# Kernel optimization log

Hardware: AMD Instinct MI355X
Metric: run time of the kernel (lower is better)

Reference implementation:

```python
import jax, jax.numpy as jnp
import numpy as np

B, S, D = 2, 2048, 1024
H = 16
HD = D // H


def setup_inputs() -> dict:
    key = jax.random.key(0)
    k1, k2, k3 = jax.random.split(key, 3)
    x = jax.random.normal(k1, (B, S, D), dtype=jnp.float32)
    # nn.Linear(d, 3d, bias=False): weight [3d, d]; y = x @ W.T
    w_qkv = jax.random.normal(k2, (3 * D, D), dtype=jnp.float32) * (D ** -0.5)
    w_out = jax.random.normal(k3, (D, D), dtype=jnp.float32) * (D ** -0.5)
    return {"x": x, "w_qkv": w_qkv, "w_out": w_out}


def reference(x, w_qkv, w_out):
    batch, seq_len, _ = x.shape
    qkv = jnp.einsum('bsd,ed->bse', x, w_qkv)  # [B,S,3D]
    q, k, v = jnp.split(qkv, 3, axis=-1)
    # [B,S,D] -> [B,H,S,HD]
    def heads(t):
        return t.reshape(batch, seq_len, H, HD).transpose(0, 2, 1, 3)
    q, k, v = heads(q), heads(k), heads(v)
    scale = HD ** -0.5
    attn = jnp.einsum('bhqd,bhkd->bhqk', q, k) * scale  # [B,H,S,S]
    causal = jnp.triu(jnp.ones((seq_len, seq_len), dtype=bool), k=1)
    attn = jnp.where(causal, -jnp.inf, attn)
    attn = jax.nn.softmax(attn, axis=-1)
    out = jnp.einsum('bhqk,bhkd->bhqd', attn, v)  # [B,H,S,HD]
    out = out.transpose(0, 2, 1, 3).reshape(batch, seq_len, D)
    return jnp.einsum('bsd,ed->bse', out, w_out)
```

## Files before the change

kernel.cpp:

```cpp
#include <hip/hip_runtime.h>

#define NUM_B 2
#define SEQ   2048
#define DIM   1024
#define NH    16
#define HD    64

typedef __attribute__((ext_vector_type(8))) short short8;
typedef __attribute__((ext_vector_type(4))) float floatx4;
typedef unsigned short us;

#define SOFTMAX_SHIFT 12.0f

__device__ __forceinline__ us f2bf(float f) {
    unsigned u = __float_as_uint(f);
    u += 0x7fffu + ((u >> 16) & 1u);
    return (us)(u >> 16);
}
__device__ __forceinline__ us f2bf_t(float f) {
    return (us)(__float_as_uint(f) >> 16);
}

#define GLD16(gptr, lptr) __builtin_amdgcn_global_load_lds( \
    (__attribute__((address_space(1))) unsigned int*)(gptr), \
    (__attribute__((address_space(3))) unsigned int*)(lptr), 16, 0, 0)

__global__ __launch_bounds__(256) void cast_all(
    const float* __restrict__ x, const float* __restrict__ wq,
    const float* __restrict__ wo, us* __restrict__ xb,
    us* __restrict__ wqb, us* __restrict__ wob)
{
    int i = blockIdx.x * 256 + threadIdx.x;
    const float* src; us* dst; int off;
    if (i < 524288)      { src = x;  dst = xb;  off = i; }
    else if (i < 917504) { src = wq; dst = wqb; off = i - 524288; }
    else                 { src = wo; dst = wob; off = i - 917504; }
    const float4* p = (const float4*)src + (size_t)off * 2;
    float4 f0 = p[0];
    float4 f1 = p[1];
    short8 v;
    v[0] = (short)f2bf(f0.x); v[1] = (short)f2bf(f0.y);
    v[2] = (short)f2bf(f0.z); v[3] = (short)f2bf(f0.w);
    v[4] = (short)f2bf(f1.x); v[5] = (short)f2bf(f1.y);
    v[6] = (short)f2bf(f1.z); v[7] = (short)f2bf(f1.w);
    *(short8*)(dst + (size_t)off * 8) = v;
}

__global__ __launch_bounds__(256, 2) void gemm_qkv(
    const us* __restrict__ A, const us* __restrict__ Bw,
    us* __restrict__ qb, us* __restrict__ kb, us* __restrict__ vt)
{
    __shared__ us As[128 * 64];
    __shared__ us Bs[128 * 64];
    const int t = threadIdx.x;
    const int lane = t & 63, w = t >> 6;
    const int l16 = lane & 15, quad = lane >> 4;
    const int wr = (w >> 1) * 64, wc = (w & 1) * 64;
    const int m0 = blockIdx.y * 128, n0 = blockIdx.x * 128;
    const int srow = lane >> 3;
    const int soff = ((lane & 7) ^ srow) << 3;
    const int rsw  = l16 & 7;

    floatx4 acc[4][4];
    #pragma unroll
    for (int i = 0; i < 4; ++i)
        #pragma unroll
        for (int j = 0; j < 4; ++j) acc[i][j] = (floatx4){0.f, 0.f, 0.f, 0.f};

    for (int k0 = 0; k0 < DIM; k0 += 64) {
        #pragma unroll
        for (int c = 0; c < 4; ++c) {
            int chunk = w * 4 + c;
            int row = chunk * 8 + srow;
            GLD16(A  + (size_t)(m0 + row) * DIM + k0 + soff, &As[chunk * 512]);
            GLD16(Bw + (size_t)(n0 + row) * DIM + k0 + soff, &Bs[chunk * 512]);
        }
        __syncthreads();
        #pragma unroll
        for (int s = 0; s < 2; ++s) {
            short8 af[4], bf[4];
            #pragma unroll
            for (int i = 0; i < 4; ++i)
                af[i] = *(const short8*)&As[(wr + i * 16 + l16) * 64 + (((s * 4 + quad) ^ rsw) << 3)];
            #pragma unroll
            for (int j = 0; j < 4; ++j)
                bf[j] = *(const short8*)&Bs[(wc + j * 16 + l16) * 64 + (((s * 4 + quad) ^ rsw) << 3)];
            #pragma unroll
            for (int i = 0; i < 4; ++i)
                #pragma unroll
                for (int j = 0; j < 4; ++j)
                    acc[i][j] = __builtin_amdgcn_mfma_f32_16x16x32_bf16(af[i], bf[j], acc[i][j], 0, 0, 0);
        }
        __syncthreads();
    }

    #pragma unroll
    for (int i = 0; i < 4; ++i) {
        #pragma unroll
        for (int j = 0; j < 4; ++j) {
            int e = n0 + wc + j * 16 + l16;
            int which = e >> 10;
            int h  = (e >> 6) & 15;
            int hd = e & 63;
            float sc = (which == 0) ? 0.125f : 1.0f;
            #pragma unroll
            for (int r = 0; r < 4; ++r) {
                int m = m0 + wr + i * 16 + quad * 4 + r;
                int b = m >> 11, s = m & 2047;
                us v = f2bf(acc[i][j][r] * sc);
                if (which == 0)      qb[((size_t)((b * NH + h) * SEQ + s) << 6) + hd] = v;
                else if (which == 1) kb[((size_t)((b * NH + h) * SEQ + s) << 6) + hd] = v;
                else                 vt[((size_t)((b * NH + h) * HD + hd) << 11) + s] = v;
            }
        }
    }
}

__global__ __launch_bounds__(256, 2) void gemm_out(
    const us* __restrict__ A, const us* __restrict__ Bw, float* __restrict__ outp)
{
    __shared__ us As[64 * 64];
    __shared__ us Bs[128 * 64];
    const int t = threadIdx.x;
    const int lane = t & 63, w = t >> 6;
    const int l16 = lane & 15, quad = lane >> 4;
    const int wr = (w >> 1) * 32, wc = (w & 1) * 64;
    const int m0 = blockIdx.y * 64, n0 = blockIdx.x * 128;
    const int srow = lane >> 3;
    const int soff = ((lane & 7) ^ srow) << 3;
    const int rsw  = l16 & 7;

    floatx4 acc[2][4];
    #pragma unroll
    for (int i = 0; i < 2; ++i)
        #pragma unroll
        for (int j = 0; j < 4; ++j) acc[i][j] = (floatx4){0.f, 0.f, 0.f, 0.f};

    for (int k0 = 0; k0 < DIM; k0 += 64) {
        #pragma unroll
        for (int c = 0; c < 2; ++c) {
            int chunk = w * 2 + c;
            int row = chunk * 8 + srow;
            GLD16(A + (size_t)(m0 + row) * DIM + k0 + soff, &As[chunk * 512]);
        }
        #pragma unroll
        for (int c = 0; c < 4; ++c) {
            int chunk = w * 4 + c;
            int row = chunk * 8 + srow;
            GLD16(Bw + (size_t)(n0 + row) * DIM + k0 + soff, &Bs[chunk * 512]);
        }
        __syncthreads();
        #pragma unroll
        for (int s = 0; s < 2; ++s) {
            short8 af[2], bf[4];
            #pragma unroll
            for (int i = 0; i < 2; ++i)
                af[i] = *(const short8*)&As[(wr + i * 16 + l16) * 64 + (((s * 4 + quad) ^ rsw) << 3)];
            #pragma unroll
            for (int j = 0; j < 4; ++j)
                bf[j] = *(const short8*)&Bs[(wc + j * 16 + l16) * 64 + (((s * 4 + quad) ^ rsw) << 3)];
            #pragma unroll
            for (int i = 0; i < 2; ++i)
                #pragma unroll
                for (int j = 0; j < 4; ++j)
                    acc[i][j] = __builtin_amdgcn_mfma_f32_16x16x32_bf16(af[i], bf[j], acc[i][j], 0, 0, 0);
        }
        __syncthreads();
    }

    #pragma unroll
    for (int i = 0; i < 2; ++i)
        #pragma unroll
        for (int j = 0; j < 4; ++j) {
            int n = n0 + wc + j * 16 + l16;
            #pragma unroll
            for (int r = 0; r < 4; ++r) {
                int m = m0 + wr + i * 16 + quad * 4 + r;
                outp[(size_t)m * DIM + n] = acc[i][j][r];
            }
        }
}

__global__ __launch_bounds__(256, 4) void attn(
    const us* __restrict__ qb, const us* __restrict__ kb,
    const us* __restrict__ vt, us* __restrict__ ob)
{
    __shared__ us Ks[64 * 64];
    __shared__ us Vs[64 * 64];
    __shared__ us Ps[4 * 16 * 72];
    const int t = threadIdx.x;
    const int lane = t & 63, w = t >> 6;
    const int l16 = lane & 15, quad = lane >> 4;
    const int idx = blockIdx.x;
    const int qt = 31 - (idx >> 5);
    const int bh = idx & 31;
    const int b = bh >> 4, h = bh & 15;
    const int q0 = qt << 6;
    const int r0 = q0 + w * 16;
    const int rowb = r0 + quad * 4;
    const size_t base = (size_t)bh * SEQ * HD;
    const us* qbh = qb + base;
    const us* kbh = kb + base;
    const us* vth = vt + base;
    us* Pp = Ps + w * 16 * 72;
    const int srow = lane >> 3;
    const int soff = ((lane & 7) ^ srow) << 3;
    const int rsw  = l16 & 7;

    short8 qa[2];
    #pragma unroll
    for (int s = 0; s < 2; ++s)
        qa[s] = *(const short8*)(qbh + (size_t)(r0 + l16) * HD + s * 32 + quad * 8);

    floatx4 o[4];
    #pragma unroll
    for (int j = 0; j < 4; ++j) o[j] = (floatx4){0.f, 0.f, 0.f, 0.f};
    float lrow[4] = {0.f, 0.f, 0.f, 0.f};

    for (int kt = 0; kt <= qt; ++kt) {
        const int j0 = kt << 6;
        #pragma unroll
        for (int c = 0; c < 2; ++c) {
            int chunk = w * 2 + c;
            int row = chunk * 8 + srow;
            GLD16(kbh + (size_t)(j0 + row) * HD + soff, &Ks[chunk * 512]);
            GLD16(vth + (size_t)row * SEQ + j0 + soff, &Vs[chunk * 512]);
        }
        __syncthreads();

        floatx4 sf[4];
        #pragma unroll
        for (int j = 0; j < 4; ++j)
            sf[j] = (floatx4){-SOFTMAX_SHIFT, -SOFTMAX_SHIFT, -SOFTMAX_SHIFT, -SOFTMAX_SHIFT};
        #pragma unroll
        for (int s = 0; s < 2; ++s)
            #pragma unroll
            for (int j = 0; j < 4; ++j) {
                short8 kf = *(const short8*)&Ks[(j * 16 + l16) * 64 + (((s * 4 + quad) ^ rsw) << 3)];
                sf[j] = __builtin_amdgcn_mfma_f32_16x16x32_bf16(qa[s], kf, sf[j], 0, 0, 0);
            }

        float p[4][4];
        #pragma unroll
        for (int j = 0; j < 4; ++j)
            #pragma unroll
            for (int r = 0; r < 4; ++r) p[j][r] = sf[j][r];

        if (kt == qt) {
            #pragma unroll
            for (int j = 0; j < 4; ++j) {
                int colg = j0 + j * 16 + l16;
                #pragma unroll
                for (int r = 0; r < 4; ++r)
                    if (colg > rowb + r) p[j][r] = -1e30f;
            }
        }

        #pragma unroll
        for (int j = 0; j < 4; ++j)
            #pragma unroll
            for (int r = 0; r < 4; ++r) {
                p[j][r] = __expf(p[j][r]);
                Pp[(quad * 4 + r) * 72 + j * 16 + l16] = f2bf_t(p[j][r]);
            }
        #pragma unroll
        for (int r = 0; r < 4; ++r)
            lrow[r] += (p[0][r] + p[1][r]) + (p[2][r] + p[3][r]);

        #pragma unroll
        for (int s = 0; s < 2; ++s) {
            short8 pf = *(const short8*)&Pp[l16 * 72 + s * 32 + quad * 8];
            #pragma unroll
            for (int j = 0; j < 4; ++j) {
                short8 vf = *(const short8*)&Vs[(j * 16 + l16) * 64 + (((s * 4 + quad) ^ rsw) << 3)];
                o[j] = __builtin_amdgcn_mfma_f32_16x16x32_bf16(pf, vf, o[j], 0, 0, 0);
            }
        }
        __syncthreads();
    }

    #pragma unroll
    for (int r = 0; r < 4; ++r) {
        float l = lrow[r];
        l += __shfl_xor(l, 1);
        l += __shfl_xor(l, 2);
        l += __shfl_xor(l, 4);
        l += __shfl_xor(l, 8);
        float inv = 1.0f / l;
        #pragma unroll
        for (int j = 0; j < 4; ++j) {
            float val = o[j][r] * inv;
            ob[(size_t)(b * SEQ + rowb + r) * DIM + h * HD + j * 16 + l16] = f2bf(val);
        }
    }
}

extern "C" void kernel_launch(void* const* d_in, const int* in_sizes, int n_in,
                              void* d_out, int out_size, void* d_ws, size_t ws_size,
                              hipStream_t stream) {
    const float* x     = (const float*)d_in[0];
    const float* w_qkv = (const float*)d_in[1];
    const float* w_out = (const float*)d_in[2];
    float* out = (float*)d_out;
    us* ws = (us*)d_ws;

    const size_t M1 = (size_t)1024 * 1024;
    us* xb  = ws;
    us* wqb = xb  + 4 * M1;
    us* wob = wqb + 3 * M1;
    us* qb  = wob + 1 * M1;
    us* kb  = qb  + 4 * M1;
    us* vt  = kb  + 4 * M1;
    us* obf = vt  + 4 * M1;

    cast_all<<<4096, 256, 0, stream>>>(x, w_qkv, w_out, xb, wqb, wob);
    gemm_qkv<<<dim3(24, 32), 256, 0, stream>>>(xb, wqb, qb, kb, vt);
    attn<<<1024, 256, 0, stream>>>(qb, kb, vt, obf);
    gemm_out<<<dim3(8, 64), 256, 0, stream>>>(obf, wob, out);
}
```

Measured before the change: 173.0 us.

## Rewrite attention with 32x32x16 MFMA and 128-row query tiles

The attention kernel now gives each block 128 query rows instead of 64, and each wave handles 32 rows using 32x32x16 bf16 MFMA in place of 16x16x32. Every K/V tile staged in LDS is therefore reused by twice as many query rows, and fewer MFMA instructions are issued per tile. Causal work is balanced by pairing tile indices across the two halves of the grid. The costs are a larger P buffer with a new swizzle, more accumulator registers with occupancy lowered to 2 blocks per CU, half as many blocks, and masking that now covers the last two key tiles.

```diff
diff --git a/kernel.cpp b/kernel.cpp
--- a/kernel.cpp
+++ b/kernel.cpp
@@ -7,7 +7,9 @@
 #define HD    64
 
 typedef __attribute__((ext_vector_type(8))) short short8;
+typedef __attribute__((ext_vector_type(4))) short short4v;
 typedef __attribute__((ext_vector_type(4))) float floatx4;
+typedef __attribute__((ext_vector_type(16))) float floatx16;
 typedef unsigned short us;
 
 #define SOFTMAX_SHIFT 12.0f
@@ -181,43 +183,46 @@
         }
 }
 
-__global__ __launch_bounds__(256, 4) void attn(
+__global__ __launch_bounds__(256, 2) void attn(
     const us* __restrict__ qb, const us* __restrict__ kb,
     const us* __restrict__ vt, us* __restrict__ ob)
 {
     __shared__ us Ks[64 * 64];
     __shared__ us Vs[64 * 64];
-    __shared__ us Ps[4 * 16 * 72];
+    __shared__ us Ps[4 * 32 * 64];
     const int t = threadIdx.x;
     const int lane = t & 63, w = t >> 6;
-    const int l16 = lane & 15, quad = lane >> 4;
+    const int l31 = lane & 31, hi = lane >> 5;
     const int idx = blockIdx.x;
-    const int qt = 31 - (idx >> 5);
-    const int bh = idx & 31;
+    const int ii = idx & 255;
+    const int Qi = (idx >> 8) ? (ii >> 5) : (15 - (ii >> 5));
+    const int bh = ii & 31;
     const int b = bh >> 4, h = bh & 15;
-    const int q0 = qt << 6;
-    const int r0 = q0 + w * 16;
-    const int rowb = r0 + quad * 4;
+    const int q0 = Qi << 7;
+    const int myrow = q0 + ((l31 >> 4) << 6) + (w << 4) + (l31 & 15);
     const size_t base = (size_t)bh * SEQ * HD;
     const us* qbh = qb + base;
     const us* kbh = kb + base;
     const us* vth = vt + base;
-    us* Pp = Ps + w * 16 * 72;
+    us* Pp = Ps + w * 32 * 64;
     const int srow = lane >> 3;
     const int soff = ((lane & 7) ^ srow) << 3;
-    const int rsw  = l16 & 7;
-
-    short8 qa[2];
-    #pragma unroll
-    for (int s = 0; s < 2; ++s)
-        qa[s] = *(const short8*)(qbh + (size_t)(r0 + l16) * HD + s * 32 + quad * 8);
-
-    floatx4 o[4];
-    #pragma unroll
-    for (int j = 0; j < 4; ++j) o[j] = (floatx4){0.f, 0.f, 0.f, 0.f};
-    float lrow[4] = {0.f, 0.f, 0.f, 0.f};
-
-    for (int kt = 0; kt <= qt; ++kt) {
+    const int xsw = l31 & 7;
+    const int nk = 2 * Qi + 2;
+
+    short8 qa[4];
+    #pragma unroll
+    for (int s = 0; s < 4; ++s)
+        qa[s] = *(const short8*)(qbh + (size_t)myrow * HD + s * 16 + hi * 8);
+
+    floatx16 o[2];
+    #pragma unroll
+    for (int db = 0; db < 2; ++db)
+        #pragma unroll
+        for (int e = 0; e < 16; ++e) o[db][e] = 0.f;
+    float lsum = 0.f;
+
+    for (int kt = 0; kt < nk; ++kt) {
         const int j0 = kt << 6;
         #pragma unroll
         for (int c = 0; c < 2; ++c) {
@@ -228,69 +233,72 @@
         }
         __syncthreads();
 
-        floatx4 sf[4];
-        #pragma unroll
-        for (int j = 0; j < 4; ++j)
-            sf[j] = (floatx4){-SOFTMAX_SHIFT, -SOFTMAX_SHIFT, -SOFTMAX_SHIFT, -SOFTMAX_SHIFT};
-        #pragma unroll
-        for (int s = 0; s < 2; ++s)
-            #pragma unroll
-            for (int j = 0; j < 4; ++j) {
-                short8 kf = *(const short8*)&Ks[(j * 16 + l16) * 64 + (((s * 4 + quad) ^ rsw) << 3)];
-                sf[j] = __builtin_amdgcn_mfma_f32_16x16x32_bf16(qa[s], kf, sf[j], 0, 0, 0);
-            }
-
-        float p[4][4];
-        #pragma unroll
-        for (int j = 0; j < 4; ++j)
-            #pragma unroll
-            for (int r = 0; r < 4; ++r) p[j][r] = sf[j][r];
-
-        if (kt == qt) {
-            #pragma unroll
-            for (int j = 0; j < 4; ++j) {
-                int colg = j0 + j * 16 + l16;
+        floatx16 sfa[2];
+        #pragma unroll
+        for (int kb2 = 0; kb2 < 2; ++kb2)
+            #pragma unroll
+            for (int e = 0; e < 16; ++e) sfa[kb2][e] = -SOFTMAX_SHIFT;
+        #pragma unroll
+        for (int kb2 = 0; kb2 < 2; ++kb2)
+            #pragma unroll
+            for (int s = 0; s < 4; ++s) {
+                short8 kf = *(const short8*)&Ks[(kb2 * 32 + l31) * 64 + (((s * 2 + hi) ^ xsw) << 3)];
+                sfa[kb2] = __builtin_amdgcn_mfma_f32_32x32x16_bf16(kf, qa[s], sfa[kb2], 0, 0, 0);
+            }
+
+        if (kt >= nk - 2) {
+            #pragma unroll
+            for (int kb2 = 0; kb2 < 2; ++kb2)
                 #pragma unroll
-                for (int r = 0; r < 4; ++r)
-                    if (colg > rowb + r) p[j][r] = -1e30f;
-            }
-        }
-
-        #pragma unroll
-        for (int j = 0; j < 4; ++j)
-            #pragma unroll
-            for (int r = 0; r < 4; ++r) {
-                p[j][r] = __expf(p[j][r]);
-                Pp[(quad * 4 + r) * 72 + j * 16 + l16] = f2bf_t(p[j][r]);
-            }
-        #pragma unroll
-        for (int r = 0; r < 4; ++r)
-            lrow[r] += (p[0][r] + p[1][r]) + (p[2][r] + p[3][r]);
-
-        #pragma unroll
-        for (int s = 0; s < 2; ++s) {
-            short8 pf = *(const short8*)&Pp[l16 * 72 + s * 32 + quad * 8];
-            #pragma unroll
-            for (int j = 0; j < 4; ++j) {
-                short8 vf = *(const short8*)&Vs[(j * 16 + l16) * 64 + (((s * 4 + quad) ^ rsw) << 3)];
-                o[j] = __builtin_amdgcn_mfma_f32_16x16x32_bf16(pf, vf, o[j], 0, 0, 0);
-            }
-        }
-        __syncthreads();
-    }
-
-    #pragma unroll
-    for (int r = 0; r < 4; ++r) {
-        float l = lrow[r];
-        l += __shfl_xor(l, 1);
-        l += __shfl_xor(l, 2);
-        l += __shfl_xor(l, 4);
-        l += __shfl_xor(l, 8);
-        float inv = 1.0f / l;
-        #pragma unroll
-        for (int j = 0; j < 4; ++j) {
-            float val = o[j][r] * inv;
-            ob[(size_t)(b * SEQ + rowb + r) * DIM + h * HD + j * 16 + l16] = f2bf(val);
+                for (int reg = 0; reg < 16; ++reg) {
+                    int key = j0 + kb2 * 32 + (reg & 3) + ((reg >> 2) << 3) + (hi << 2);
+                    if (key > myrow) sfa[kb2][reg] = -1e30f;
+                }
+        }
+
+        #pragma unroll
+        for (int kb2 = 0; kb2 < 2; ++kb2) {
+            float pv[16];
+            #pragma unroll
+            for (int reg = 0; reg < 16; ++reg) {
+                pv[reg] = __expf(sfa[kb2][reg]);
+                lsum += pv[reg];
+            }
+            #pragma unroll
+            for (int rg = 0; rg < 4; ++rg) {
+                short4v pk;
+                pk[0] = (short)f2bf_t(pv[rg * 4 + 0]);
+                pk[1] = (short)f2bf_t(pv[rg * 4 + 1]);
+                pk[2] = (short)f2bf_t(pv[rg * 4 + 2]);
+                pk[3] = (short)f2bf_t(pv[rg * 4 + 3]);
+                *(short4v*)&Pp[l31 * 64 + (((kb2 * 4 + rg) ^ xsw) << 3) + (hi << 2)] = pk;
+            }
+        }
+
+        short8 pf[4];
+        #pragma unroll
+        for (int kc = 0; kc < 4; ++kc)
+            pf[kc] = *(const short8*)&Pp[l31 * 64 + (((kc * 2 + hi) ^ xsw) << 3)];
+        #pragma unroll
+        for (int db = 0; db < 2; ++db)
+            #pragma unroll
+            for (int kc = 0; kc < 4; ++kc) {
+                short8 vf = *(const short8*)&Vs[(db * 32 + l31) * 64 + (((kc * 2 + hi) ^ xsw) << 3)];
+                o[db] = __builtin_amdgcn_mfma_f32_32x32x16_bf16(pf[kc], vf, o[db], 0, 0, 0);
+            }
+        __syncthreads();
+    }
+
+    lsum += __shfl_xor(lsum, 32);
+    #pragma unroll
+    for (int reg = 0; reg < 16; ++reg) {
+        int rr = (reg & 3) + ((reg >> 2) << 3) + (hi << 2);
+        float linv = 1.0f / __shfl(lsum, rr);
+        int grow = q0 + ((rr >> 4) << 6) + (w << 4) + (rr & 15);
+        #pragma unroll
+        for (int db = 0; db < 2; ++db) {
+            int d = db * 32 + l31;
+            ob[(size_t)(b * SEQ + grow) * DIM + h * HD + d] = f2bf(o[db][reg] * linv);
         }
     }
 }
@@ -315,6 +323,6 @@
 
     cast_all<<<4096, 256, 0, stream>>>(x, w_qkv, w_out, xb, wqb, wob);
     gemm_qkv<<<dim3(24, 32), 256, 0, stream>>>(xb, wqb, qb, kb, vt);
-    attn<<<1024, 256, 0, stream>>>(qb, kb, vt, obf);
+    attn<<<512, 256, 0, stream>>>(qb, kb, vt, obf);
     gemm_out<<<dim3(8, 64), 256, 0, stream>>>(obf, wob, out);
 }
```

New measurement: 181.2 us. +4.7%, slower.

## Double-buffer K/V tiles in attention and transpose V accumulation for coalesced stores

Applied to the files above, without the earlier changes.

The attention kernel now prefetches the next K/V tile into a second LDS buffer while computing on the current one, removing the load-then-sync stall per iteration. In the QKV GEMM, blocks producing V swap MFMA operands so accumulators hold V transposed, letting lanes write consecutive sequence positions into the vt layout. The double buffer doubles K/V LDS usage, which may reduce blocks per CU.

```diff
diff --git a/kernel.cpp b/kernel.cpp
--- a/kernel.cpp
+++ b/kernel.cpp
@@ -57,6 +57,7 @@
     const int l16 = lane & 15, quad = lane >> 4;
     const int wr = (w >> 1) * 64, wc = (w & 1) * 64;
     const int m0 = blockIdx.y * 128, n0 = blockIdx.x * 128;
+    const bool isV = (blockIdx.x >= 16);
     const int srow = lane >> 3;
     const int soff = ((lane & 7) ^ srow) << 3;
     const int rsw  = l16 & 7;
@@ -85,32 +86,56 @@
             #pragma unroll
             for (int j = 0; j < 4; ++j)
                 bf[j] = *(const short8*)&Bs[(wc + j * 16 + l16) * 64 + (((s * 4 + quad) ^ rsw) << 3)];
-            #pragma unroll
-            for (int i = 0; i < 4; ++i)
-                #pragma unroll
-                for (int j = 0; j < 4; ++j)
-                    acc[i][j] = __builtin_amdgcn_mfma_f32_16x16x32_bf16(af[i], bf[j], acc[i][j], 0, 0, 0);
-        }
-        __syncthreads();
-    }
-
-    #pragma unroll
-    for (int i = 0; i < 4; ++i) {
-        #pragma unroll
-        for (int j = 0; j < 4; ++j) {
-            int e = n0 + wc + j * 16 + l16;
-            int which = e >> 10;
-            int h  = (e >> 6) & 15;
-            int hd = e & 63;
-            float sc = (which == 0) ? 0.125f : 1.0f;
-            #pragma unroll
-            for (int r = 0; r < 4; ++r) {
-                int m = m0 + wr + i * 16 + quad * 4 + r;
-                int b = m >> 11, s = m & 2047;
-                us v = f2bf(acc[i][j][r] * sc);
-                if (which == 0)      qb[((size_t)((b * NH + h) * SEQ + s) << 6) + hd] = v;
-                else if (which == 1) kb[((size_t)((b * NH + h) * SEQ + s) << 6) + hd] = v;
-                else                 vt[((size_t)((b * NH + h) * HD + hd) << 11) + s] = v;
+            if (!isV) {
+                #pragma unroll
+                for (int i = 0; i < 4; ++i)
+                    #pragma unroll
+                    for (int j = 0; j < 4; ++j)
+                        acc[i][j] = __builtin_amdgcn_mfma_f32_16x16x32_bf16(af[i], bf[j], acc[i][j], 0, 0, 0);
+            } else {
+                #pragma unroll
+                for (int i = 0; i < 4; ++i)
+                    #pragma unroll
+                    for (int j = 0; j < 4; ++j)
+                        acc[i][j] = __builtin_amdgcn_mfma_f32_16x16x32_bf16(bf[j], af[i], acc[i][j], 0, 0, 0);
+            }
+        }
+        __syncthreads();
+    }
+
+    if (!isV) {
+        const int which = n0 >> 10;
+        const float sc = (which == 0) ? 0.125f : 1.0f;
+        us* dst = (which == 0) ? qb : kb;
+        #pragma unroll
+        for (int i = 0; i < 4; ++i) {
+            #pragma unroll
+            for (int j = 0; j < 4; ++j) {
+                int e = n0 + wc + j * 16 + l16;
+                int h  = (e >> 6) & 15;
+                int hd = e & 63;
+                #pragma unroll
+                for (int r = 0; r < 4; ++r) {
+                    int m = m0 + wr + i * 16 + quad * 4 + r;
+                    int b = m >> 11, s = m & 2047;
+                    dst[((size_t)((b * NH + h) * SEQ + s) << 6) + hd] = f2bf(acc[i][j][r] * sc);
+                }
+            }
+        }
+    } else {
+        #pragma unroll
+        for (int i = 0; i < 4; ++i) {
+            int m = m0 + wr + i * 16 + l16;
+            int b = m >> 11, s = m & 2047;
+            #pragma unroll
+            for (int j = 0; j < 4; ++j) {
+                int e0 = (n0 - 2048) + wc + j * 16 + quad * 4;
+                #pragma unroll
+                for (int r = 0; r < 4; ++r) {
+                    int e = e0 + r;
+                    int h = e >> 6, hd = e & 63;
+                    vt[((size_t)((b * NH + h) * HD + hd) << 11) + s] = f2bf(acc[i][j][r]);
+                }
             }
         }
     }
@@ -185,8 +210,8 @@
     const us* __restrict__ qb, const us* __restrict__ kb,
     const us* __restrict__ vt, us* __restrict__ ob)
 {
-    __shared__ us Ks[64 * 64];
-    __shared__ us Vs[64 * 64];
+    __shared__ us Ks[2][64 * 64];
+    __shared__ us Vs[2][64 * 64];
     __shared__ us Ps[4 * 16 * 72];
     const int t = threadIdx.x;
     const int lane = t & 63, w = t >> 6;
@@ -217,16 +242,27 @@
     for (int j = 0; j < 4; ++j) o[j] = (floatx4){0.f, 0.f, 0.f, 0.f};
     float lrow[4] = {0.f, 0.f, 0.f, 0.f};
 
+    #pragma unroll
+    for (int c = 0; c < 2; ++c) {
+        int chunk = w * 2 + c;
+        int row = chunk * 8 + srow;
+        GLD16(kbh + (size_t)row * HD + soff, &Ks[0][chunk * 512]);
+        GLD16(vth + (size_t)row * SEQ + soff, &Vs[0][chunk * 512]);
+    }
+    __syncthreads();
+
     for (int kt = 0; kt <= qt; ++kt) {
-        const int j0 = kt << 6;
-        #pragma unroll
-        for (int c = 0; c < 2; ++c) {
-            int chunk = w * 2 + c;
-            int row = chunk * 8 + srow;
-            GLD16(kbh + (size_t)(j0 + row) * HD + soff, &Ks[chunk * 512]);
-            GLD16(vth + (size_t)row * SEQ + j0 + soff, &Vs[chunk * 512]);
-        }
-        __syncthreads();
+        const int cur = kt & 1;
+        if (kt < qt) {
+            const int j0n = (kt + 1) << 6;
+            #pragma unroll
+            for (int c = 0; c < 2; ++c) {
+                int chunk = w * 2 + c;
+                int row = chunk * 8 + srow;
+                GLD16(kbh + (size_t)(j0n + row) * HD + soff, &Ks[cur ^ 1][chunk * 512]);
+                GLD16(vth + (size_t)row * SEQ + j0n + soff, &Vs[cur ^ 1][chunk * 512]);
+            }
+        }
 
         floatx4 sf[4];
         #pragma unroll
@@ -236,7 +272,7 @@
         for (int s = 0; s < 2; ++s)
             #pragma unroll
             for (int j = 0; j < 4; ++j) {
-                short8 kf = *(const short8*)&Ks[(j * 16 + l16) * 64 + (((s * 4 + quad) ^ rsw) << 3)];
+                short8 kf = *(const short8*)&Ks[cur][(j * 16 + l16) * 64 + (((s * 4 + quad) ^ rsw) << 3)];
                 sf[j] = __builtin_amdgcn_mfma_f32_16x16x32_bf16(qa[s], kf, sf[j], 0, 0, 0);
             }
 
@@ -247,6 +283,7 @@
             for (int r = 0; r < 4; ++r) p[j][r] = sf[j][r];
 
         if (kt == qt) {
+            const int j0 = kt << 6;
             #pragma unroll
             for (int j = 0; j < 4; ++j) {
                 int colg = j0 + j * 16 + l16;
@@ -272,7 +309,7 @@
             short8 pf = *(const short8*)&Pp[l16 * 72 + s * 32 + quad * 8];
             #pragma unroll
             for (int j = 0; j < 4; ++j) {
-                short8 vf = *(const short8*)&Vs[(j * 16 + l16) * 64 + (((s * 4 + quad) ^ rsw) << 3)];
+                short8 vf = *(const short8*)&Vs[cur][(j * 16 + l16) * 64 + (((s * 4 + quad) ^ rsw) << 3)];
                 o[j] = __builtin_amdgcn_mfma_f32_16x16x32_bf16(pf, vf, o[j], 0, 0, 0);
             }
         }
```

After: 170.3 us. About the same (-1.6%).
